# Optimization experiments

Hardware: AMD Instinct MI355X
Metric: run time of the kernel (lower is better)

The kernel has to match this reference:

```python
import jax, jax.numpy as jnp
import numpy as np

NUM_HEADS = 8
NEG_INF = -1e9  # stand-in for -inf in the causal mask (avoids nan under masked softmax)


def setup_inputs() -> dict:
    key = jax.random.key(0)
    ks = jax.random.split(key, 8)
    B, C, H, W = 2, 512, 64, 64
    E = 512
    s = 1.0 / np.sqrt(C)
    return {
        "query": jax.random.normal(ks[0], (B, C, H, W), jnp.float32),
        "key": jax.random.normal(ks[1], (B, C, H, W), jnp.float32),
        "Wq": jax.random.normal(ks[2], (E, C), jnp.float32) * s,
        "bq": jax.random.normal(ks[3], (E,), jnp.float32) * 0.01,
        "Wk": jax.random.normal(ks[4], (E, C), jnp.float32) * s,
        "bk": jax.random.normal(ks[5], (E,), jnp.float32) * 0.01,
        "Wv": jax.random.normal(ks[6], (E, C), jnp.float32) * s,
        "bv": jax.random.normal(ks[7], (E,), jnp.float32) * 0.01,
    }


def reference(query, key, Wq, bq, Wk, bk, Wv, bv):
    B, qdim, H, W = query.shape
    N = H * W
    E = Wq.shape[0]
    nh = NUM_HEADS
    hd = E // nh

    # (B, C, H, W) -> (B, N, C)
    q_tok = query.transpose(0, 2, 3, 1).reshape(B, N, qdim)
    k_tok = key.transpose(0, 2, 3, 1).reshape(B, N, key.shape[1])

    q = (q_tok @ Wq.T + bq).reshape(B, N, nh, hd)
    k = (k_tok @ Wk.T + bk).reshape(B, N, nh, hd)
    v = (k_tok @ Wv.T + bv).reshape(B, N, nh, hd)

    # scores: (B, heads, N, N)
    scores = jnp.einsum("bqhd,bkhd->bhqk", q, k) / jnp.sqrt(jnp.float32(hd))
    causal = jnp.tril(jnp.ones((N, N), dtype=bool))
    scores = jnp.where(causal, scores, NEG_INF)
    attn = jax.nn.softmax(scores, axis=-1)  # dropout p=0.0 -> identity

    x = jnp.einsum("bhqk,bkhd->bhqd", attn, v)  # (B, h, N, hd)
    # permute to (B, h, hd, N) then view as (B, E, H, W) — matches torch ordering
    out = x.transpose(0, 1, 3, 2).reshape(B, E, H, W)
    return out
```

## Files before the change

kernel.cpp:

```cpp
#include <hip/hip_runtime.h>


typedef __bf16 bf16;
typedef __attribute__((ext_vector_type(8))) __bf16 bf16x8;
typedef __attribute__((ext_vector_type(4))) float floatx4;

#define B_ 2
#define Cc 512
#define Nn 4096
#define Ee 512
#define NH 8
#define HD 64

#define QSCALE 0.1803368801111204f

__global__ __launch_bounds__(64) void detect_dtype(
    const unsigned short* __restrict__ w, int* __restrict__ flag) {
  bool bad = false;
#pragma unroll
  for (int i = 0; i < 16; ++i) {
    unsigned u = w[threadIdx.x * 16 + i];
    float v = __uint_as_float(u << 16);
    bad |= !(v > -1024.f && v < 1024.f);
  }
  unsigned long long b = __ballot(bad);
  if (threadIdx.x == 0) *flag = (b != 0ull) ? 1 : 0;
}

#define WSEG 262144
#define WTOT 787968
__global__ __launch_bounds__(256) void wcvt(
    const float* __restrict__ Wq, const float* __restrict__ Wk,
    const float* __restrict__ Wv, const float* __restrict__ bq,
    const float* __restrict__ bk, const float* __restrict__ bv,
    bf16* __restrict__ out, const int* __restrict__ flagp) {
  if (!*flagp) return;
  int idx = (blockIdx.x * 256 + threadIdx.x) * 8;
  if (idx >= WTOT) return;
  const float* src;
  int off;
  if (idx < WSEG)            { src = Wq; off = idx; }
  else if (idx < 2 * WSEG)   { src = Wk; off = idx - WSEG; }
  else if (idx < 3 * WSEG)   { src = Wv; off = idx - 2 * WSEG; }
  else if (idx < 3 * WSEG + 512)  { src = bq; off = idx - 3 * WSEG; }
  else if (idx < 3 * WSEG + 1024) { src = bk; off = idx - 3 * WSEG - 512; }
  else                            { src = bv; off = idx - 3 * WSEG - 1024; }
  float4 a = *(const float4*)(src + off);
  float4 c = *(const float4*)(src + off + 4);
  union { bf16 h[8]; bf16x8 v; } u;
  u.h[0] = (bf16)a.x; u.h[1] = (bf16)a.y; u.h[2] = (bf16)a.z; u.h[3] = (bf16)a.w;
  u.h[4] = (bf16)c.x; u.h[5] = (bf16)c.y; u.h[6] = (bf16)c.z; u.h[7] = (bf16)c.w;
  *(bf16x8*)(out + idx) = u.v;
}

__device__ __forceinline__ bf16x8 load8e(const void* base, size_t eidx, int f32) {
  if (!f32) return *(const bf16x8*)((const bf16*)base + eidx);
  const float* f = (const float*)base + eidx;
  float4 a = *(const float4*)f;
  float4 c = *(const float4*)(f + 4);
  union { bf16 h[8]; bf16x8 v; } u;
  u.h[0] = (bf16)a.x; u.h[1] = (bf16)a.y; u.h[2] = (bf16)a.z; u.h[3] = (bf16)a.w;
  u.h[4] = (bf16)c.x; u.h[5] = (bf16)c.y; u.h[6] = (bf16)c.z; u.h[7] = (bf16)c.w;
  return u.v;
}

__global__ __launch_bounds__(256) void transpose_k(
    const void* __restrict__ X0, const void* __restrict__ X1,
    bf16* __restrict__ T0, bf16* __restrict__ T1,
    const int* __restrict__ flagp) {
  const int f32 = *flagp;
  __shared__ __align__(16) bf16 T[64 * 64];
  const int z = blockIdx.z;
  const int bb = z & 1;
  const void* src = (z >> 1) ? X1 : X0;
  bf16* dst = (z >> 1) ? T1 : T0;
  const int n0 = blockIdx.x * 64, c0 = blockIdx.y * 64;
  const int t = threadIdx.x;
  const size_t sbase = ((size_t)bb * Cc + c0) * (size_t)Nn + n0;

#pragma unroll
  for (int it = 0; it < 2; ++it) {
    int task = t + it * 256;
    int crow = task >> 3, gr = task & 7;
    bf16x8 v = load8e(src, sbase + (size_t)crow * Nn + gr * 8, f32);
    int slot = gr ^ (crow & 7);
    *(bf16x8*)&T[crow * 64 + slot * 8] = v;
  }
  __syncthreads();
  const int nrow = t & 63, cp = t >> 6;
  bf16* db = dst + ((size_t)bb * Nn + n0 + nrow) * Cc + c0;
#pragma unroll
  for (int it = 0; it < 2; ++it) {
    int cg = cp * 2 + it;
    union { bf16 h[8]; bf16x8 v; } u;
#pragma unroll
    for (int j = 0; j < 8; ++j) {
      int c = cg * 8 + j;
      int slot = (nrow >> 3) ^ (c & 7);
      u.h[j] = T[c * 64 + slot * 8 + (nrow & 7)];
    }
    *(bf16x8*)(db + cg * 8) = u.v;
  }
}

__global__ __launch_bounds__(256) void gemm3(
    const bf16* __restrict__ Xtq, const bf16* __restrict__ Xtk,
    const void* __restrict__ Wq0, const bf16* __restrict__ Wqb,
    const void* __restrict__ Wk0, const bf16* __restrict__ Wkb,
    const void* __restrict__ Wv0, const bf16* __restrict__ Wvb,
    const void* __restrict__ bq0, const bf16* __restrict__ bqb,
    const void* __restrict__ bk0, const bf16* __restrict__ bkb,
    const void* __restrict__ bv0, const bf16* __restrict__ bvb,
    bf16* __restrict__ Qt, bf16* __restrict__ Kt, bf16* __restrict__ Vh,
    int zoff, const int* __restrict__ flagp) {
  const int f32 = *flagp;
  const int z = (int)blockIdx.z + zoff;
  const int op = z >> 1, b = z & 1;
  const bf16 *A, *Bt, *bias;
  bf16* Out;
  long sAb, sBb, sOb;
  int Nq, biasOnM, m0, n0;
  float scaleOut;
  if (op == 0) {
    A = Xtq; sAb = (long)Nn * Cc;
    Bt = f32 ? Wqb : (const bf16*)Wq0; sBb = 0;
    bias = f32 ? bqb : (const bf16*)bq0;
    Out = Qt; sOb = (long)Nn * Ee; Nq = Ee; biasOnM = 0; scaleOut = QSCALE;
    m0 = blockIdx.x * 128; n0 = blockIdx.y * 64;
  } else if (op == 1) {
    A = Xtk; sAb = (long)Nn * Cc;
    Bt = f32 ? Wkb : (const bf16*)Wk0; sBb = 0;
    bias = f32 ? bkb : (const bf16*)bk0;
    Out = Kt; sOb = (long)Nn * Ee; Nq = Ee; biasOnM = 0; scaleOut = 1.0f;
    m0 = blockIdx.x * 128; n0 = blockIdx.y * 64;
  } else {
    A = f32 ? Wvb : (const bf16*)Wv0; sAb = 0;
    Bt = Xtk; sBb = (long)Nn * Cc;
    bias = f32 ? bvb : (const bf16*)bv0;
    Out = Vh; sOb = (long)Ee * Nn; Nq = Nn; biasOnM = 1; scaleOut = 1.0f;
    m0 = (blockIdx.x >> 3) * 128;
    n0 = (blockIdx.y * 8 + (blockIdx.x & 7)) * 64;
  }
  constexpr int K = 512;
  constexpr int SA = 40;
  __shared__ __align__(16) bf16 As[2][128 * SA];
  __shared__ __align__(16) bf16 Bs[2][64 * SA];
  const int tid = threadIdx.x;
  const int lane = tid & 63, wave = tid >> 6;
  const int quad = lane >> 4, lm = lane & 15;
  const bf16* Ab = A + (size_t)b * sAb;
  const bf16* Bb = Bt + (size_t)b * sBb;
  bf16* Ob = Out + (size_t)b * sOb;

  const int arow = tid >> 2, ag = tid & 3;

  floatx4 acc[2][4];
#pragma unroll
  for (int i = 0; i < 2; ++i)
#pragma unroll
    for (int j = 0; j < 4; ++j) acc[i][j] = (floatx4){0.f, 0.f, 0.f, 0.f};

  bf16x8 a0 = *(const bf16x8*)(Ab + (size_t)(m0 + arow) * K + ag * 8);
  bf16x8 a1 = *(const bf16x8*)(Ab + (size_t)(m0 + 64 + arow) * K + ag * 8);
  bf16x8 b0 = *(const bf16x8*)(Bb + (size_t)(n0 + arow) * K + ag * 8);
  *(bf16x8*)&As[0][arow * SA + ag * 8] = a0;
  *(bf16x8*)&As[0][(64 + arow) * SA + ag * 8] = a1;
  *(bf16x8*)&Bs[0][arow * SA + ag * 8] = b0;
  __syncthreads();

  for (int kk = 0; kk < 16; ++kk) {
    const int c = kk & 1;
    const bool more = kk < 15;
    if (more) {
      int k0 = (kk + 1) * 32;
      a0 = *(const bf16x8*)(Ab + (size_t)(m0 + arow) * K + k0 + ag * 8);
      a1 = *(const bf16x8*)(Ab + (size_t)(m0 + 64 + arow) * K + k0 + ag * 8);
      b0 = *(const bf16x8*)(Bb + (size_t)(n0 + arow) * K + k0 + ag * 8);
    }
    bf16x8 af[2], bfr[4];
#pragma unroll
    for (int mf = 0; mf < 2; ++mf) {
      int r = wave * 32 + mf * 16 + lm;
      af[mf] = *(const bf16x8*)&As[c][r * SA + quad * 8];
    }
#pragma unroll
    for (int nf = 0; nf < 4; ++nf) {
      int r = nf * 16 + lm;
      bfr[nf] = *(const bf16x8*)&Bs[c][r * SA + quad * 8];
    }
    if (more) {
      *(bf16x8*)&As[c ^ 1][arow * SA + ag * 8] = a0;
      *(bf16x8*)&As[c ^ 1][(64 + arow) * SA + ag * 8] = a1;
      *(bf16x8*)&Bs[c ^ 1][arow * SA + ag * 8] = b0;
    }
#pragma unroll
    for (int mf = 0; mf < 2; ++mf)
#pragma unroll
      for (int nf = 0; nf < 4; ++nf)
        acc[mf][nf] = __builtin_amdgcn_mfma_f32_16x16x32_bf16(
            af[mf], bfr[nf], acc[mf][nf], 0, 0, 0);
    __syncthreads();
  }

#pragma unroll
  for (int mf = 0; mf < 2; ++mf) {
#pragma unroll
    for (int nf = 0; nf < 4; ++nf) {
      int col = n0 + nf * 16 + lm;
      float bn = biasOnM ? 0.f : (float)bias[col];
#pragma unroll
      for (int r = 0; r < 4; ++r) {
        int rowg = m0 + wave * 32 + mf * 16 + quad * 4 + r;
        float bv = biasOnM ? (float)bias[rowg] : bn;
        float val = (acc[mf][nf][r] + bv) * scaleOut;
        if (!biasOnM) {
          Ob[(size_t)rowg * Nq + col] = (bf16)val;
        } else {
          int hh = rowg >> 6, dd = rowg & 63;
          int dfv = dd >> 4, dl = dd & 15;
          int ktl = col >> 6, kkv = col & 63;
          int g2 = kkv >> 5, q8 = (kkv >> 3) & 3, jv = kkv & 7;
          size_t idxv = ((size_t)hh * 262144) +
                        ((((size_t)ktl * 8 + g2 * 4 + dfv) * 64 +
                          q8 * 16 + dl) * 8 + jv);
          Ob[idxv] = (bf16)val;
        }
      }
    }
  }
}

__device__ __forceinline__ float fast_exp2(float x) {
  return __builtin_amdgcn_exp2f(x);
}
__device__ __forceinline__ unsigned pack_bf16_2(float a, float b) {
  unsigned ua = __float_as_uint(a) + 0x8000u;
  unsigned ub = __float_as_uint(b) + 0x8000u;
  return (ua >> 16) | (ub & 0xFFFF0000u);
}

__global__ __launch_bounds__(256, 4) void attn(
    const bf16* __restrict__ Qt, const bf16* __restrict__ Kt,
    const bf16* __restrict__ Ve, void* __restrict__ Out,
    const int* __restrict__ flagp) {
  const int f32 = *flagp;
  constexpr int SK = 72;
  __shared__ __align__(16) bf16 Ks[2][64 * SK];
  const int tid = threadIdx.x, lane = tid & 63, w = tid >> 6;
  const int quad = lane >> 4, lm = lane & 15;

  const int L = (int)blockIdx.x + 64 * (int)blockIdx.y + 512 * (int)blockIdx.z;
  const int xcd = L & 7, slot0 = L >> 3;
  const int half = slot0 >> 6, sp = slot0 & 63;
  const int p = half ? 63 - sp : sp;
  const int hp = xcd * 2 + half;
  const int b = hp >> 3, h = hp & 7;

  const int Q0 = p * 64;
  const int qbase = Q0 + w * 16;
  const int last = p;

  bf16x8 qf[2];
  {
    const bf16* qp =
        Qt + ((size_t)b * Nn + qbase + lm) * Ee + h * HD + quad * 8;
    qf[0] = *(const bf16x8*)qp;
    qf[1] = *(const bf16x8*)(qp + 32);
  }
  floatx4 accO[4];
#pragma unroll
  for (int df = 0; df < 4; ++df) accO[df] = (floatx4){0.f, 0.f, 0.f, 0.f};
  float lsum = 0.f;

  const int r0 = tid >> 3, g = tid & 7;
  const int sslot = ((g + r0) & 7) * 8;
  const bf16* kp0 = Kt + ((size_t)b * Nn + r0) * Ee + h * HD + g * 8;
  const bf16* kp1 = kp0 + (size_t)32 * Ee;

  const bf16* Vbase =
      Ve + (size_t)b * ((size_t)Ee * Nn) + (size_t)h * 262144 + lane * 8;

  const int rbase = ((lm >> 2) << 3) | (lm & 3);

  bf16x8 ka[2], kb[2];
#define LOADK(s)                                                   \
  do {                                                             \
    ka[s] = *(const bf16x8*)kp0; kb[s] = *(const bf16x8*)kp1;      \
    kp0 += (size_t)64 * Ee; kp1 += (size_t)64 * Ee;                \
  } while (0)
#define STAGEK(s, buf)                                             \
  do {                                                             \
    *(bf16x8*)&Ks[buf][r0 * SK + sslot] = ka[s];                   \
    *(bf16x8*)&Ks[buf][(r0 + 32) * SK + sslot] = kb[s];            \
  } while (0)

  LOADK(0);
  if (last >= 1) LOADK(1);
  STAGEK(0, 0);
  __syncthreads();

#pragma unroll 1
  for (int kt = 0; kt <= last; kt += 2) {
#pragma unroll
    for (int u = 0; u < 2; ++u) {
      const int t = kt + u;
      if (u == 1 && t > last) break;
      const int k0 = t * 64;
      if (t + 2 <= last) LOADK(u);
      const bool skip = k0 > qbase + 15;

      bf16x8 pb[2];
      bf16x8 av0, av1, av2, av3, av4, av5, av6, av7;
      if (!skip) {
        floatx4 accS[4];
#pragma unroll
        for (int f = 0; f < 4; ++f) accS[f] = (floatx4){0.f, 0.f, 0.f, 0.f};
        __builtin_amdgcn_s_setprio(1);
#pragma unroll
        for (int ks = 0; ks < 2; ++ks)
#pragma unroll
          for (int f = 0; f < 4; ++f) {
            const int R = rbase + ((f & 1) << 2) + ((f >> 1) << 5);
            const int sl = (ks * 4 + quad + R) & 7;
            bf16x8 ak = *(const bf16x8*)&Ks[u][R * SK + sl * 8];
            accS[f] = __builtin_amdgcn_mfma_f32_16x16x32_bf16(
                ak, qf[ks], accS[f], 0, 0, 0);
          }
        __builtin_amdgcn_s_setprio(0);
        {
          const bf16* vt = Vbase + (size_t)t * 4096;
          av0 = *(const bf16x8*)(vt);
          av1 = *(const bf16x8*)(vt + 512);
          av2 = *(const bf16x8*)(vt + 1024);
          av3 = *(const bf16x8*)(vt + 1536);
          av4 = *(const bf16x8*)(vt + 2048);
          av5 = *(const bf16x8*)(vt + 2560);
          av6 = *(const bf16x8*)(vt + 3072);
          av7 = *(const bf16x8*)(vt + 3584);
        }
        const bool maskt = (k0 + 63 > qbase);
        if (!maskt) {
          float la = 0.f, lb = 0.f;
#pragma unroll
          for (int g2 = 0; g2 < 2; ++g2) {
            union { unsigned pk[4]; bf16x8 v; } uu;
#pragma unroll
            for (int jp = 0; jp < 4; ++jp) {
              const int fidx = g2 * 2 + (jp >> 1);
              const int re = (jp & 1) * 2;
              float p0 = fast_exp2(accS[fidx][re]);
              float p1 = fast_exp2(accS[fidx][re + 1]);
              la += p0; lb += p1;
              uu.pk[jp] = pack_bf16_2(p0, p1);
            }
            pb[g2] = uu.v;
          }
          lsum += la + lb;
        } else {
          const int qg = qbase + lm;
          float la = 0.f, lb = 0.f;
#pragma unroll
          for (int g2 = 0; g2 < 2; ++g2) {
            union { unsigned pk[4]; bf16x8 v; } uu;
#pragma unroll
            for (int jp = 0; jp < 4; ++jp) {
              const int fidx = g2 * 2 + (jp >> 1);
              const int re = (jp & 1) * 2;
              const int key0 = k0 + g2 * 32 + quad * 8 + jp * 2;
              float p0 = fast_exp2(accS[fidx][re]);
              float p1 = fast_exp2(accS[fidx][re + 1]);
              if (key0 > qg) p0 = 0.f;
              if (key0 + 1 > qg) p1 = 0.f;
              la += p0; lb += p1;
              uu.pk[jp] = pack_bf16_2(p0, p1);
            }
            pb[g2] = uu.v;
          }
          lsum += la + lb;
        }
      }
      if (t + 1 <= last) STAGEK(u ^ 1, u ^ 1);
      if (!skip) {
        __builtin_amdgcn_s_setprio(1);
        accO[0] = __builtin_amdgcn_mfma_f32_16x16x32_bf16(av0, pb[0], accO[0], 0, 0, 0);
        accO[1] = __builtin_amdgcn_mfma_f32_16x16x32_bf16(av1, pb[0], accO[1], 0, 0, 0);
        accO[2] = __builtin_amdgcn_mfma_f32_16x16x32_bf16(av2, pb[0], accO[2], 0, 0, 0);
        accO[3] = __builtin_amdgcn_mfma_f32_16x16x32_bf16(av3, pb[0], accO[3], 0, 0, 0);
        accO[0] = __builtin_amdgcn_mfma_f32_16x16x32_bf16(av4, pb[1], accO[0], 0, 0, 0);
        accO[1] = __builtin_amdgcn_mfma_f32_16x16x32_bf16(av5, pb[1], accO[1], 0, 0, 0);
        accO[2] = __builtin_amdgcn_mfma_f32_16x16x32_bf16(av6, pb[1], accO[2], 0, 0, 0);
        accO[3] = __builtin_amdgcn_mfma_f32_16x16x32_bf16(av7, pb[1], accO[3], 0, 0, 0);
        __builtin_amdgcn_s_setprio(0);
      }
      __syncthreads();
    }
  }
#undef LOADK
#undef STAGEK

  lsum += __shfl_xor(lsum, 16);
  lsum += __shfl_xor(lsum, 32);

  const float inv = 1.0f / lsum;
  const int qg = qbase + lm;
#pragma unroll
  for (int df = 0; df < 4; ++df) {
#pragma unroll
    for (int r = 0; r < 4; ++r) {
      int d = h * HD + df * 16 + quad * 4 + r;
      size_t off = ((size_t)b * Ee + d) * Nn + qg;
      if (!f32) ((bf16*)Out)[off] = (bf16)(accO[df][r] * inv);
      else      ((float*)Out)[off] = accO[df][r] * inv;
    }
  }
}

extern "C" void kernel_launch(void* const* d_in, const int* in_sizes, int n_in,
                              void* d_out, int out_size, void* d_ws,
                              size_t ws_size, hipStream_t stream) {
  const void* q  = d_in[0];
  const void* k  = d_in[1];
  const void* Wq = d_in[2];
  const void* bq = d_in[3];
  const void* Wk = d_in[4];
  const void* bk = d_in[5];
  const void* Wv = d_in[6];
  const void* bv = d_in[7];

  const size_t SZ = (size_t)B_ * Nn * Cc;
  int*  flag = (int*)d_ws;
  bf16* Xtq  = (bf16*)((char*)d_ws + 1024);
  bf16* Qt   = Xtq + SZ;
  bf16* Kt   = Qt + SZ;
  bf16* Xtk  = (bf16*)d_out;
  bf16* Vh   = Xtq;
  bf16* Wb   = (bf16*)((char*)d_out + 8 * 1024 * 1024);
  bf16* Wqb = Wb,            *Wkb = Wb + WSEG,    *Wvb = Wb + 2 * WSEG;
  bf16* bqb = Wb + 3 * WSEG, *bkb = bqb + 512,    *bvb = bqb + 1024;

  detect_dtype<<<1, 64, 0, stream>>>((const unsigned short*)Wq, flag);
  wcvt<<<(WTOT / 8 + 255) / 256, 256, 0, stream>>>(
      (const float*)Wq, (const float*)Wk, (const float*)Wv,
      (const float*)bq, (const float*)bk, (const float*)bv, Wb, flag);
  transpose_k<<<dim3(64, 8, 4), 256, 0, stream>>>(q, k, Xtq, Xtk, flag);
  gemm3<<<dim3(32, 8, 4), 256, 0, stream>>>(
      Xtq, Xtk, Wq, Wqb, Wk, Wkb, Wv, Wvb,
      bq, bqb, bk, bkb, bv, bvb, Qt, Kt, Vh, 0, flag);
  gemm3<<<dim3(32, 8, 2), 256, 0, stream>>>(
      Xtq, Xtk, Wq, Wqb, Wk, Wkb, Wv, Wvb,
      bq, bqb, bk, bkb, bv, bvb, Qt, Kt, Vh, 4, flag);
  attn<<<dim3(64, NH, B_), 256, 0, stream>>>(Qt, Kt, Vh, d_out, flag);
}
```

Measured before the change: 199.9 us.

## Write K in MFMA-fragment layout and load it directly, dropping LDS staging

The projection GEMM now writes K in a per-head, MFMA-fragment-ordered layout, as was already done for V. The attention kernel then reads K fragments straight from global memory with contiguous per-lane vector loads, which removes the shared-memory double buffer and the per-tile __syncthreads. Block-to-work mapping also changes: each XCD gets one head, and query tiles are ordered so causal work balances across slots. The trade-off is that every wave re-reads K from global/L2 instead of sharing one LDS copy per block, and K-load latency is no longer hidden by explicit prefetch. The skip check for fully masked tiles is also gone, which is fine here because the block's tile count is exactly its causal range.

Measured after the change: 206.3 us. +3.2%, slower.

```diff
diff --git a/kernel.cpp b/kernel.cpp
--- a/kernel.cpp
+++ b/kernel.cpp
@@ -119,25 +119,28 @@
   const bf16 *A, *Bt, *bias;
   bf16* Out;
   long sAb, sBb, sOb;
-  int Nq, biasOnM, m0, n0;
+  int Nq, biasOnM, m0, n0, outMode;
   float scaleOut;
   if (op == 0) {
     A = Xtq; sAb = (long)Nn * Cc;
     Bt = f32 ? Wqb : (const bf16*)Wq0; sBb = 0;
     bias = f32 ? bqb : (const bf16*)bq0;
     Out = Qt; sOb = (long)Nn * Ee; Nq = Ee; biasOnM = 0; scaleOut = QSCALE;
+    outMode = 0;
     m0 = blockIdx.x * 128; n0 = blockIdx.y * 64;
   } else if (op == 1) {
     A = Xtk; sAb = (long)Nn * Cc;
     Bt = f32 ? Wkb : (const bf16*)Wk0; sBb = 0;
     bias = f32 ? bkb : (const bf16*)bk0;
     Out = Kt; sOb = (long)Nn * Ee; Nq = Ee; biasOnM = 0; scaleOut = 1.0f;
+    outMode = 1;
     m0 = blockIdx.x * 128; n0 = blockIdx.y * 64;
   } else {
     A = f32 ? Wvb : (const bf16*)Wv0; sAb = 0;
     Bt = Xtk; sBb = (long)Nn * Cc;
     bias = f32 ? bvb : (const bf16*)bv0;
     Out = Vh; sOb = (long)Ee * Nn; Nq = Nn; biasOnM = 1; scaleOut = 1.0f;
+    outMode = 2;
     m0 = (blockIdx.x >> 3) * 128;
     n0 = (blockIdx.y * 8 + (blockIdx.x & 7)) * 64;
   }
@@ -213,17 +216,25 @@
         int rowg = m0 + wave * 32 + mf * 16 + quad * 4 + r;
         float bv = biasOnM ? (float)bias[rowg] : bn;
         float val = (acc[mf][nf][r] + bv) * scaleOut;
-        if (!biasOnM) {
+        if (outMode == 0) {
           Ob[(size_t)rowg * Nq + col] = (bf16)val;
+        } else if (outMode == 1) {
+          int kt = rowg >> 6, k6 = rowg & 63;
+          int lmv = (((k6 >> 3) & 3) << 2) | (k6 & 3);
+          int fv  = ((k6 >> 5) << 1) | ((k6 >> 2) & 1);
+          int hh = col >> 6, d = col & 63;
+          int ksv = d >> 5, qv = (d >> 3) & 3, jv = d & 7;
+          size_t idx = (size_t)hh * 262144 +
+                       ((size_t)(kt * 8 + fv * 2 + ksv) * 64 + qv * 16 + lmv) * 8 + jv;
+          Ob[idx] = (bf16)val;
         } else {
           int hh = rowg >> 6, dd = rowg & 63;
           int dfv = dd >> 4, dl = dd & 15;
           int ktl = col >> 6, kkv = col & 63;
           int g2 = kkv >> 5, q8 = (kkv >> 3) & 3, jv = kkv & 7;
-          size_t idxv = ((size_t)hh * 262144) +
-                        ((((size_t)ktl * 8 + g2 * 4 + dfv) * 64 +
-                          q8 * 16 + dl) * 8 + jv);
-          Ob[idxv] = (bf16)val;
+          size_t idx = (size_t)hh * 262144 +
+                       ((size_t)(ktl * 8 + g2 * 4 + dfv) * 64 + q8 * 16 + dl) * 8 + jv;
+          Ob[idx] = (bf16)val;
         }
       }
     }
@@ -244,21 +255,16 @@
     const bf16* __restrict__ Ve, void* __restrict__ Out,
     const int* __restrict__ flagp) {
   const int f32 = *flagp;
-  constexpr int SK = 72;
-  __shared__ __align__(16) bf16 Ks[2][64 * SK];
   const int tid = threadIdx.x, lane = tid & 63, w = tid >> 6;
   const int quad = lane >> 4, lm = lane & 15;
 
   const int L = (int)blockIdx.x + 64 * (int)blockIdx.y + 512 * (int)blockIdx.z;
-  const int xcd = L & 7, slot0 = L >> 3;
-  const int half = slot0 >> 6, sp = slot0 & 63;
-  const int p = half ? 63 - sp : sp;
-  const int hp = xcd * 2 + half;
-  const int b = hp >> 3, h = hp & 7;
-
-  const int Q0 = p * 64;
-  const int qbase = Q0 + w * 16;
-  const int last = p;
+  const int xcd = L & 7, slot = L >> 3;
+  const int i = slot & 31, k4 = slot >> 5;
+  const int h = xcd, b = i >> 4, m = i & 15;
+  const int p = (k4 == 0) ? m : (k4 == 1) ? 31 - m : (k4 == 2) ? 32 + m : 63 - m;
+
+  const int qbase = p * 64 + w * 16;
 
   bf16x8 qf[2];
   {
@@ -272,131 +278,101 @@
   for (int df = 0; df < 4; ++df) accO[df] = (floatx4){0.f, 0.f, 0.f, 0.f};
   float lsum = 0.f;
 
-  const int r0 = tid >> 3, g = tid & 7;
-  const int sslot = ((g + r0) & 7) * 8;
-  const bf16* kp0 = Kt + ((size_t)b * Nn + r0) * Ee + h * HD + g * 8;
-  const bf16* kp1 = kp0 + (size_t)32 * Ee;
-
-  const bf16* Vbase =
-      Ve + (size_t)b * ((size_t)Ee * Nn) + (size_t)h * 262144 + lane * 8;
-
-  const int rbase = ((lm >> 2) << 3) | (lm & 3);
-
-  bf16x8 ka[2], kb[2];
-#define LOADK(s)                                                   \
-  do {                                                             \
-    ka[s] = *(const bf16x8*)kp0; kb[s] = *(const bf16x8*)kp1;      \
-    kp0 += (size_t)64 * Ee; kp1 += (size_t)64 * Ee;                \
-  } while (0)
-#define STAGEK(s, buf)                                             \
-  do {                                                             \
-    *(bf16x8*)&Ks[buf][r0 * SK + sslot] = ka[s];                   \
-    *(bf16x8*)&Ks[buf][(r0 + 32) * SK + sslot] = kb[s];            \
-  } while (0)
-
-  LOADK(0);
-  if (last >= 1) LOADK(1);
-  STAGEK(0, 0);
-  __syncthreads();
+  const bf16* kb =
+      Kt + (size_t)b * ((size_t)Nn * Ee) + (size_t)h * 262144 + lane * 8;
+  const bf16* vb =
+      Ve + (size_t)b * ((size_t)Nn * Ee) + (size_t)h * 262144 + lane * 8;
 
 #pragma unroll 1
-  for (int kt = 0; kt <= last; kt += 2) {
-#pragma unroll
-    for (int u = 0; u < 2; ++u) {
-      const int t = kt + u;
-      if (u == 1 && t > last) break;
-      const int k0 = t * 64;
-      if (t + 2 <= last) LOADK(u);
-      const bool skip = k0 > qbase + 15;
-
-      bf16x8 pb[2];
-      bf16x8 av0, av1, av2, av3, av4, av5, av6, av7;
-      if (!skip) {
-        floatx4 accS[4];
-#pragma unroll
-        for (int f = 0; f < 4; ++f) accS[f] = (floatx4){0.f, 0.f, 0.f, 0.f};
-        __builtin_amdgcn_s_setprio(1);
-#pragma unroll
-        for (int ks = 0; ks < 2; ++ks)
-#pragma unroll
-          for (int f = 0; f < 4; ++f) {
-            const int R = rbase + ((f & 1) << 2) + ((f >> 1) << 5);
-            const int sl = (ks * 4 + quad + R) & 7;
-            bf16x8 ak = *(const bf16x8*)&Ks[u][R * SK + sl * 8];
-            accS[f] = __builtin_amdgcn_mfma_f32_16x16x32_bf16(
-                ak, qf[ks], accS[f], 0, 0, 0);
-          }
-        __builtin_amdgcn_s_setprio(0);
-        {
-          const bf16* vt = Vbase + (size_t)t * 4096;
-          av0 = *(const bf16x8*)(vt);
-          av1 = *(const bf16x8*)(vt + 512);
-          av2 = *(const bf16x8*)(vt + 1024);
-          av3 = *(const bf16x8*)(vt + 1536);
-          av4 = *(const bf16x8*)(vt + 2048);
-          av5 = *(const bf16x8*)(vt + 2560);
-          av6 = *(const bf16x8*)(vt + 3072);
-          av7 = *(const bf16x8*)(vt + 3584);
+  for (int t = 0; t <= p; ++t) {
+    bf16x8 kf0 = *(const bf16x8*)(kb);
+    bf16x8 kf1 = *(const bf16x8*)(kb + 512);
+    bf16x8 kf2 = *(const bf16x8*)(kb + 1024);
+    bf16x8 kf3 = *(const bf16x8*)(kb + 1536);
+    bf16x8 kf4 = *(const bf16x8*)(kb + 2048);
+    bf16x8 kf5 = *(const bf16x8*)(kb + 2560);
+    bf16x8 kf6 = *(const bf16x8*)(kb + 3072);
+    bf16x8 kf7 = *(const bf16x8*)(kb + 3584);
+    kb += 4096;
+
+    floatx4 accS[4];
+#pragma unroll
+    for (int f = 0; f < 4; ++f) accS[f] = (floatx4){0.f, 0.f, 0.f, 0.f};
+    __builtin_amdgcn_s_setprio(1);
+    accS[0] = __builtin_amdgcn_mfma_f32_16x16x32_bf16(kf0, qf[0], accS[0], 0, 0, 0);
+    accS[0] = __builtin_amdgcn_mfma_f32_16x16x32_bf16(kf1, qf[1], accS[0], 0, 0, 0);
+    accS[1] = __builtin_amdgcn_mfma_f32_16x16x32_bf16(kf2, qf[0], accS[1], 0, 0, 0);
+    accS[1] = __builtin_amdgcn_mfma_f32_16x16x32_bf16(kf3, qf[1], accS[1], 0, 0, 0);
+    accS[2] = __builtin_amdgcn_mfma_f32_16x16x32_bf16(kf4, qf[0], accS[2], 0, 0, 0);
+    accS[2] = __builtin_amdgcn_mfma_f32_16x16x32_bf16(kf5, qf[1], accS[2], 0, 0, 0);
+    accS[3] = __builtin_amdgcn_mfma_f32_16x16x32_bf16(kf6, qf[0], accS[3], 0, 0, 0);
+    accS[3] = __builtin_amdgcn_mfma_f32_16x16x32_bf16(kf7, qf[1], accS[3], 0, 0, 0);
+    __builtin_amdgcn_s_setprio(0);
+
+    bf16x8 av0 = *(const bf16x8*)(vb);
+    bf16x8 av1 = *(const bf16x8*)(vb + 512);
+    bf16x8 av2 = *(const bf16x8*)(vb + 1024);
+    bf16x8 av3 = *(const bf16x8*)(vb + 1536);
+    bf16x8 av4 = *(const bf16x8*)(vb + 2048);
+    bf16x8 av5 = *(const bf16x8*)(vb + 2560);
+    bf16x8 av6 = *(const bf16x8*)(vb + 3072);
+    bf16x8 av7 = *(const bf16x8*)(vb + 3584);
+    vb += 4096;
+
+    bf16x8 pb[2];
+    const int k0 = t * 64;
+    const bool maskt = (k0 + 63 > qbase);
+    if (!maskt) {
+      float la = 0.f, lb = 0.f;
+#pragma unroll
+      for (int g2 = 0; g2 < 2; ++g2) {
+        union { unsigned pk[4]; bf16x8 v; } uu;
+#pragma unroll
+        for (int jp = 0; jp < 4; ++jp) {
+          const int fidx = g2 * 2 + (jp >> 1);
+          const int re = (jp & 1) * 2;
+          float p0 = fast_exp2(accS[fidx][re]);
+          float p1 = fast_exp2(accS[fidx][re + 1]);
+          la += p0; lb += p1;
+          uu.pk[jp] = pack_bf16_2(p0, p1);
         }
-        const bool maskt = (k0 + 63 > qbase);
-        if (!maskt) {
-          float la = 0.f, lb = 0.f;
-#pragma unroll
-          for (int g2 = 0; g2 < 2; ++g2) {
-            union { unsigned pk[4]; bf16x8 v; } uu;
-#pragma unroll
-            for (int jp = 0; jp < 4; ++jp) {
-              const int fidx = g2 * 2 + (jp >> 1);
-              const int re = (jp & 1) * 2;
-              float p0 = fast_exp2(accS[fidx][re]);
-              float p1 = fast_exp2(accS[fidx][re + 1]);
-              la += p0; lb += p1;
-              uu.pk[jp] = pack_bf16_2(p0, p1);
-            }
-            pb[g2] = uu.v;
-          }
-          lsum += la + lb;
-        } else {
-          const int qg = qbase + lm;
-          float la = 0.f, lb = 0.f;
-#pragma unroll
-          for (int g2 = 0; g2 < 2; ++g2) {
-            union { unsigned pk[4]; bf16x8 v; } uu;
-#pragma unroll
-            for (int jp = 0; jp < 4; ++jp) {
-              const int fidx = g2 * 2 + (jp >> 1);
-              const int re = (jp & 1) * 2;
-              const int key0 = k0 + g2 * 32 + quad * 8 + jp * 2;
-              float p0 = fast_exp2(accS[fidx][re]);
-              float p1 = fast_exp2(accS[fidx][re + 1]);
-              if (key0 > qg) p0 = 0.f;
-              if (key0 + 1 > qg) p1 = 0.f;
-              la += p0; lb += p1;
-              uu.pk[jp] = pack_bf16_2(p0, p1);
-            }
-            pb[g2] = uu.v;
-          }
-          lsum += la + lb;
+        pb[g2] = uu.v;
+      }
+      lsum += la + lb;
+    } else {
+      const int qg = qbase + lm;
+      float la = 0.f, lb = 0.f;
+#pragma unroll
+      for (int g2 = 0; g2 < 2; ++g2) {
+        union { unsigned pk[4]; bf16x8 v; } uu;
+#pragma unroll
+        for (int jp = 0; jp < 4; ++jp) {
+          const int fidx = g2 * 2 + (jp >> 1);
+          const int re = (jp & 1) * 2;
+          const int key0 = k0 + g2 * 32 + quad * 8 + jp * 2;
+          float p0 = fast_exp2(accS[fidx][re]);
+          float p1 = fast_exp2(accS[fidx][re + 1]);
+          if (key0 > qg) p0 = 0.f;
+          if (key0 + 1 > qg) p1 = 0.f;
+          la += p0; lb += p1;
+          uu.pk[jp] = pack_bf16_2(p0, p1);
         }
+        pb[g2] = uu.v;
       }
-      if (t + 1 <= last) STAGEK(u ^ 1, u ^ 1);
-      if (!skip) {
-        __builtin_amdgcn_s_setprio(1);
-        accO[0] = __builtin_amdgcn_mfma_f32_16x16x32_bf16(av0, pb[0], accO[0], 0, 0, 0);
-        accO[1] = __builtin_amdgcn_mfma_f32_16x16x32_bf16(av1, pb[0], accO[1], 0, 0, 0);
-        accO[2] = __builtin_amdgcn_mfma_f32_16x16x32_bf16(av2, pb[0], accO[2], 0, 0, 0);
-        accO[3] = __builtin_amdgcn_mfma_f32_16x16x32_bf16(av3, pb[0], accO[3], 0, 0, 0);
-        accO[0] = __builtin_amdgcn_mfma_f32_16x16x32_bf16(av4, pb[1], accO[0], 0, 0, 0);
-        accO[1] = __builtin_amdgcn_mfma_f32_16x16x32_bf16(av5, pb[1], accO[1], 0, 0, 0);
-        accO[2] = __builtin_amdgcn_mfma_f32_16x16x32_bf16(av6, pb[1], accO[2], 0, 0, 0);
-        accO[3] = __builtin_amdgcn_mfma_f32_16x16x32_bf16(av7, pb[1], accO[3], 0, 0, 0);
-        __builtin_amdgcn_s_setprio(0);
-      }
-      __syncthreads();
-    }
-  }
-#undef LOADK
-#undef STAGEK
+      lsum += la + lb;
+    }
+
+    __builtin_amdgcn_s_setprio(1);
+    accO[0] = __builtin_amdgcn_mfma_f32_16x16x32_bf16(av0, pb[0], accO[0], 0, 0, 0);
+    accO[1] = __builtin_amdgcn_mfma_f32_16x16x32_bf16(av1, pb[0], accO[1], 0, 0, 0);
+    accO[2] = __builtin_amdgcn_mfma_f32_16x16x32_bf16(av2, pb[0], accO[2], 0, 0, 0);
+    accO[3] = __builtin_amdgcn_mfma_f32_16x16x32_bf16(av3, pb[0], accO[3], 0, 0, 0);
+    accO[0] = __builtin_amdgcn_mfma_f32_16x16x32_bf16(av4, pb[1], accO[0], 0, 0, 0);
+    accO[1] = __builtin_amdgcn_mfma_f32_16x16x32_bf16(av5, pb[1], accO[1], 0, 0, 0);
+    accO[2] = __builtin_amdgcn_mfma_f32_16x16x32_bf16(av6, pb[1], accO[2], 0, 0, 0);
+    accO[3] = __builtin_amdgcn_mfma_f32_16x16x32_bf16(av7, pb[1], accO[3], 0, 0, 0);
+    __builtin_amdgcn_s_setprio(0);
+  }
 
   lsum += __shfl_xor(lsum, 16);
   lsum += __shfl_xor(lsum, 32);
```
